# Performance work log

Measured on AMD Instinct MI355X. Metric: run time of the kernel, lower is better.

Reference implementation:

```python
import jax, jax.numpy as jnp
import numpy as np

B, T, C = 16, 2048, 64  # embed_size = 64 (module constant); block_size = T
HEAD = 64


def setup_inputs() -> dict:
    key = jax.random.key(0)
    kx, kq, kk, kv = jax.random.split(key, 4)
    x = jax.random.normal(kx, (B, T, C), dtype=jnp.float32)
    # nn.Linear(embed_size, head_size, bias=False) weights: shape [head_size, embed_size]
    s = 1.0 / np.sqrt(C)
    Wq = jax.random.uniform(kq, (HEAD, C), dtype=jnp.float32, minval=-s, maxval=s)
    Wk = jax.random.uniform(kk, (HEAD, C), dtype=jnp.float32, minval=-s, maxval=s)
    Wv = jax.random.uniform(kv, (HEAD, C), dtype=jnp.float32, minval=-s, maxval=s)
    return {"x": x, "Wq": Wq, "Wk": Wk, "Wv": Wv}


def reference(x, Wq, Wk, Wv):
    Bx, Tx, Cx = x.shape
    q = jnp.einsum('btc,hc->bth', x, Wq)  # [B,T,HEAD]
    k = jnp.einsum('btc,hc->bth', x, Wk)
    v = jnp.einsum('btc,hc->bth', x, Wv)
    scale = Cx ** -0.5  # NOTE: source scales by embed dim C, not head_size
    wei = jnp.einsum('bth,bsh->bts', q, k) * scale  # [B,T,T]
    causal = jnp.tril(jnp.ones((Tx, Tx), dtype=bool))
    wei = jnp.where(causal, wei, -jnp.inf)
    wei = jax.nn.softmax(wei, axis=-1)
    out = jnp.einsum('bts,bsh->bth', wei, v)  # [B,T,HEAD]
    return out
```

## Files before the change

kernel.cpp:

```cpp
#include <hip/hip_runtime.h>


#define Bsz 16
#define Tsz 2048
#define LOG2E 1.44269504088896340736f
#define MFIX 12.0f

typedef __attribute__((ext_vector_type(8))) short bf16x8;
typedef __attribute__((ext_vector_type(4))) short bf16x4;
typedef __attribute__((ext_vector_type(4))) float f32x4;

__device__ inline unsigned short f2bf(float f) {
  union { float f; unsigned u; } v; v.f = f;
  unsigned r = v.u + 0x7fffu + ((v.u >> 16) & 1u);
  return (unsigned short)(r >> 16);
}

__device__ inline bf16x8 pack8(const float* f, float s) {
  bf16x8 o;
#pragma unroll
  for (int i = 0; i < 8; i++) o[i] = (short)f2bf(f[i] * s);
  return o;
}

__device__ inline unsigned pack2_rtz(float a, float b) {
  union { float f; unsigned u; } ua, ub; ua.f = a; ub.f = b;
  return (ua.u >> 16) | (ub.u & 0xffff0000u);
}

__device__ inline float ex2(float x) {
#if __has_builtin(__builtin_amdgcn_exp2f)
  return __builtin_amdgcn_exp2f(x);
#else
  return exp2f(x);
#endif
}

__device__ inline f32x4 pv_mfma(bf16x4 a, bf16x4 b, f32x4 c) {
#if __has_builtin(__builtin_amdgcn_mfma_f32_16x16x16bf16_1k)
  return __builtin_amdgcn_mfma_f32_16x16x16bf16_1k(a, b, c, 0, 0, 0);
#else
  bf16x8 av = {a[0], a[1], a[2], a[3], 0, 0, 0, 0};
  bf16x8 bv = {b[0], b[1], b[2], b[3], 0, 0, 0, 0};
  return __builtin_amdgcn_mfma_f32_16x16x32_bf16(av, bv, c, 0, 0, 0);
#endif
}

__device__ inline void gload_lds16(const unsigned short* g, unsigned short* l) {
  __builtin_amdgcn_global_load_lds(
      (const __attribute__((address_space(1))) unsigned int*)(g),
      (__attribute__((address_space(3))) unsigned int*)(l), 16, 0, 0);
}

__global__ __launch_bounds__(256) void proj_kernel(
    const float* __restrict__ x, const float* __restrict__ Wq,
    const float* __restrict__ Wk, const float* __restrict__ Wv,
    unsigned short* __restrict__ Qs, unsigned short* __restrict__ Kg,
    unsigned short* __restrict__ Vg) {
  __shared__ unsigned short Xb[64 * 72];
  const int b = blockIdx.y, t = blockIdx.x, tbase = t * 64, tid = threadIdx.x;
  const int lane = tid & 63, w = tid >> 6, l15 = lane & 15, quad = lane >> 4;

  bf16x8 bw[3][4][2];
  const float* Ws[3] = {Wq, Wk, Wv};
#pragma unroll
  for (int m = 0; m < 3; m++) {
    const float sc = (m == 0) ? 0.125f * LOG2E : 1.0f;
#pragma unroll
    for (int nb = 0; nb < 4; nb++) {
      const float* wp = Ws[m] + (nb * 16 + l15) * 64 + quad * 8;
      float tf[8];
#pragma unroll
      for (int i = 0; i < 8; i++) tf[i] = wp[i];
      bw[m][nb][0] = pack8(tf, sc);
#pragma unroll
      for (int i = 0; i < 8; i++) tf[i] = wp[32 + i];
      bw[m][nb][1] = pack8(tf, sc);
    }
  }
  {
    const int r = tid >> 2, c0 = (tid & 3) * 16;
    const float* xp = x + ((size_t)b * Tsz + tbase + r) * 64 + c0;
    float tf[16];
#pragma unroll
    for (int i = 0; i < 4; i++) {
      float4 v = *(const float4*)(xp + i * 4);
      tf[i * 4 + 0] = v.x; tf[i * 4 + 1] = v.y; tf[i * 4 + 2] = v.z; tf[i * 4 + 3] = v.w;
    }
    unsigned short* dst = &Xb[r * 72 + c0];
    *(bf16x8*)dst = pack8(tf, 1.0f);
    *(bf16x8*)(dst + 8) = pack8(tf + 8, 1.0f);
  }
  __syncthreads();

  const unsigned short* ap = &Xb[(w * 16 + l15) * 72 + quad * 8];
  const bf16x8 a0 = *(const bf16x8*)ap;
  const bf16x8 a1 = *(const bf16x8*)(ap + 32);

  f32x4 acc[3][4];
#pragma unroll
  for (int m = 0; m < 3; m++)
#pragma unroll
    for (int nb = 0; nb < 4; nb++) {
      f32x4 c = (f32x4){0.f, 0.f, 0.f, 0.f};
      c = __builtin_amdgcn_mfma_f32_16x16x32_bf16(a0, bw[m][nb][0], c, 0, 0, 0);
      c = __builtin_amdgcn_mfma_f32_16x16x32_bf16(a1, bw[m][nb][1], c, 0, 0, 0);
      acc[m][nb] = c;
    }
#pragma unroll
  for (int nb = 0; nb < 4; nb++)
#pragma unroll
    for (int r = 0; r < 4; r++) {
      const size_t row = (size_t)b * Tsz + tbase + w * 16 + quad * 4 + r;
      Qs[row * 64 + nb * 16 + l15] = f2bf(acc[0][nb][r]);
    }
  __syncthreads();
#pragma unroll
  for (int nb = 0; nb < 4; nb++)
#pragma unroll
    for (int r = 0; r < 4; r++)
      Xb[(w * 16 + quad * 4 + r) * 72 + nb * 16 + l15] = f2bf(acc[1][nb][r]);
  __syncthreads();
  const size_t img = ((size_t)b * 32 + t) * 4096;
#pragma unroll
  for (int i = 0; i < 2; i++) {
    const int c = tid + i * 256;
    const int nb = c >> 7, rem = c & 127;
    const int half = rem >> 6, ln = rem & 63;
    const int lr = ln & 15, lq = ln >> 4;
    bf16x8 v = *(const bf16x8*)&Xb[(nb * 16 + lr) * 72 + half * 32 + lq * 8];
    *(bf16x8*)(Kg + img + c * 8) = v;
  }
  __syncthreads();
#pragma unroll
  for (int nb = 0; nb < 4; nb++)
#pragma unroll
    for (int r = 0; r < 4; r++)
      Xb[(nb * 16 + l15) * 72 + quad * 16 + w * 4 + r] = f2bf(acc[2][nb][r]);
  __syncthreads();
#pragma unroll
  for (int i = 0; i < 2; i++) {
    const int c = tid + i * 256;
    const int mb = c >> 7, rem = c & 127;
    const int plane = rem >> 6, ln = rem & 63;
    const int lr = ln & 15, lq = ln >> 4;
    bf16x8 v = *(const bf16x8*)&Xb[(mb * 16 + lr) * 72 + lq * 16 + plane * 8];
    *(bf16x8*)(Vg + img + c * 8) = v;
  }
}

__global__ __launch_bounds__(256) void flash_kernel(
    const unsigned short* __restrict__ Qs, const unsigned short* __restrict__ Kg,
    const unsigned short* __restrict__ Vg, unsigned short* __restrict__ Opart,
    float* __restrict__ Ml) {
  const int b = blockIdx.y;
  const int idx = blockIdx.x;
  int g = 0, base = 0;
  while (idx >= base + 8 * (g + 1)) { base += 8 * (g + 1); g++; }
  const int within = idx - base;
  const int qt = 8 * g + within / (g + 1);
  const int c = within % (g + 1);
  const int qbase = qt * 64;
  const int kstart = c * 512;
  const int kend = min(kstart + 512, qbase + 64);
  const int ntiles = (kend - kstart) >> 6;
  const int t0 = kstart >> 6;

  const int tid = threadIdx.x;
  const int lane = tid & 63, w = tid >> 6;
  const int l15 = lane & 15, quad = lane >> 4;
  const size_t bT = (size_t)b * Tsz;
  const int q = qbase + w * 16 + l15;

  __shared__ unsigned short buf[2][8192];

  const size_t imgbase = (size_t)b * 32 * 4096;
  const int half = (w & 1);
  const unsigned short* gsrc0 =
      ((w < 2) ? Kg : Vg) + imgbase + half * 2048 + lane * 8;
  unsigned short* ldst0 = &buf[0][(w >= 2 ? 4096 : 0) + half * 2048];

  {
    const unsigned short* s = gsrc0 + (size_t)t0 * 4096;
#pragma unroll
    for (int j = 0; j < 4; j++) gload_lds16(s + j * 512, ldst0 + j * 512);
  }

  const unsigned short* Qp = Qs + (bT + q) * 64 + quad * 8;
  const bf16x8 q0 = *(const bf16x8*)Qp;
  const bf16x8 q1 = *(const bf16x8*)(Qp + 32);

  f32x4 O[4];
#pragma unroll
  for (int mb = 0; mb < 4; mb++) O[mb] = (f32x4){0.f, 0.f, 0.f, 0.f};
  float l_acc = 0.f;

  __syncthreads();

  for (int i = 0; i < ntiles; i++) {
    const unsigned short* kb = buf[i & 1];
    const unsigned short* vb = buf[i & 1] + 4096;
    if (i + 1 < ntiles) {
      const unsigned short* s = gsrc0 + (size_t)(t0 + i + 1) * 4096;
      unsigned short* d = ldst0 + ((i + 1) & 1) * 8192;
#pragma unroll
      for (int j = 0; j < 4; j++) gload_lds16(s + j * 512, d + j * 512);
    }
    bf16x8 k0[4], k1[4];
#pragma unroll
    for (int nb = 0; nb < 4; nb++) {
      k0[nb] = *(const bf16x8*)(kb + nb * 1024 + lane * 8);
      k1[nb] = *(const bf16x8*)(kb + nb * 1024 + 512 + lane * 8);
    }
    bf16x4 vf[4][4];
#pragma unroll
    for (int mb = 0; mb < 4; mb++) {
      bf16x8 va = *(const bf16x8*)(vb + mb * 1024 + lane * 8);
      bf16x8 vb2 = *(const bf16x8*)(vb + mb * 1024 + 512 + lane * 8);
      vf[mb][0] = (bf16x4){va[0], va[1], va[2], va[3]};
      vf[mb][1] = (bf16x4){va[4], va[5], va[6], va[7]};
      vf[mb][2] = (bf16x4){vb2[0], vb2[1], vb2[2], vb2[3]};
      vf[mb][3] = (bf16x4){vb2[4], vb2[5], vb2[6], vb2[7]};
    }
    f32x4 S[4];
#pragma unroll
    for (int nb = 0; nb < 4; nb++) {
      f32x4 cc = (f32x4){0.f, 0.f, 0.f, 0.f};
      cc = __builtin_amdgcn_mfma_f32_16x16x32_bf16(k0[nb], q0, cc, 0, 0, 0);
      cc = __builtin_amdgcn_mfma_f32_16x16x32_bf16(k1[nb], q1, cc, 0, 0, 0);
      S[nb] = cc;
    }
    const int kt = kstart + i * 64;
    float p[4][4];
    if (kt == qbase) {
#pragma unroll
      for (int nb = 0; nb < 4; nb++)
#pragma unroll
        for (int r = 0; r < 4; r++) {
          const int s = kt + nb * 16 + quad * 4 + r;
          float pv = ex2(S[nb][r] - MFIX);
          p[nb][r] = (s > q) ? 0.f : pv;
        }
    } else {
#pragma unroll
      for (int nb = 0; nb < 4; nb++)
#pragma unroll
        for (int r = 0; r < 4; r++) p[nb][r] = ex2(S[nb][r] - MFIX);
    }
#pragma unroll
    for (int nb = 0; nb < 4; nb++)
#pragma unroll
      for (int r = 0; r < 4; r++) l_acc += p[nb][r];
    bf16x4 pf[4];
#pragma unroll
    for (int nb = 0; nb < 4; nb++) {
      union { unsigned u[2]; bf16x4 v; } tt;
      tt.u[0] = pack2_rtz(p[nb][0], p[nb][1]);
      tt.u[1] = pack2_rtz(p[nb][2], p[nb][3]);
      pf[nb] = tt.v;
    }
#pragma unroll
    for (int nb = 0; nb < 4; nb++)
#pragma unroll
      for (int mb = 0; mb < 4; mb++) O[mb] = pv_mfma(vf[mb][nb], pf[nb], O[mb]);
    __syncthreads();
  }

  const int pidx = b * 80 + idx;
  unsigned short* Op = Opart + (size_t)pidx * 4096 + (w * 16 + l15) * 64 + quad * 4;
#pragma unroll
  for (int mb = 0; mb < 4; mb++) {
    union { unsigned u[2]; bf16x4 v; } tt;
    tt.u[0] = (unsigned)f2bf(O[mb][0]) | ((unsigned)f2bf(O[mb][1]) << 16);
    tt.u[1] = (unsigned)f2bf(O[mb][2]) | ((unsigned)f2bf(O[mb][3]) << 16);
    *(bf16x4*)(Op + mb * 16) = tt.v;
  }
  l_acc += __shfl_xor(l_acc, 16, 64);
  l_acc += __shfl_xor(l_acc, 32, 64);
  if (quad == 0) Ml[(size_t)pidx * 64 + w * 16 + l15] = l_acc;
}

__global__ __launch_bounds__(256) void merge_kernel(
    const unsigned short* __restrict__ Opart, const float* __restrict__ Ml,
    float* __restrict__ out) {
  const int qt = blockIdx.x, b = blockIdx.y;
  const int g = qt >> 3;
  const int pbase = b * 80 + 4 * g * (g + 1) + (qt - 8 * g) * (g + 1);
  const int nch = g + 1;
  const int tid = threadIdx.x;
  const int ql = tid >> 2;
  const int h0 = (tid & 3) * 16;

  float acc[16];
#pragma unroll
  for (int i = 0; i < 16; i++) acc[i] = 0.f;
  float ld = 0.f;
  for (int c = 0; c < nch; c++) {
    const int pidx = pbase + c;
    ld += Ml[(size_t)pidx * 64 + ql];
    const unsigned short* Op = Opart + (size_t)pidx * 4096 + ql * 64 + h0;
    bf16x8 v0 = *(const bf16x8*)Op;
    bf16x8 v1 = *(const bf16x8*)(Op + 8);
#pragma unroll
    for (int i = 0; i < 8; i++) {
      union { unsigned u; float f; } t;
      t.u = ((unsigned)(unsigned short)v0[i]) << 16;
      acc[i] += t.f;
      t.u = ((unsigned)(unsigned short)v1[i]) << 16;
      acc[8 + i] += t.f;
    }
  }
  const float rd = 1.0f / ld;
  float* op = out + ((size_t)b * Tsz + qt * 64 + ql) * 64 + h0;
#pragma unroll
  for (int i = 0; i < 4; i++) {
    f32x4 v = {acc[i * 4] * rd, acc[i * 4 + 1] * rd, acc[i * 4 + 2] * rd,
               acc[i * 4 + 3] * rd};
    *(f32x4*)(op + i * 4) = v;
  }
}

extern "C" void kernel_launch(void* const* d_in, const int* in_sizes, int n_in,
                              void* d_out, int out_size, void* d_ws, size_t ws_size,
                              hipStream_t stream) {
  const float* x = (const float*)d_in[0];
  const float* Wq = (const float*)d_in[1];
  const float* Wk = (const float*)d_in[2];
  const float* Wv = (const float*)d_in[3];

  unsigned short* Qs = (unsigned short*)d_ws;
  unsigned short* Kg = Qs + (size_t)Bsz * Tsz * 64;
  unsigned short* Vg = Kg + (size_t)Bsz * Tsz * 64;
  unsigned short* Opart = Vg + (size_t)Bsz * Tsz * 64;
  float* Ml = (float*)(Opart + (size_t)Bsz * 80 * 4096);

  dim3 pgrid(Tsz / 64, Bsz);
  proj_kernel<<<pgrid, 256, 0, stream>>>(x, Wq, Wk, Wv, Qs, Kg, Vg);
  dim3 fgrid(80, Bsz);
  flash_kernel<<<fgrid, 256, 0, stream>>>(Qs, Kg, Vg, Opart, Ml);
  dim3 mgrid(32, Bsz);
  merge_kernel<<<mgrid, 256, 0, stream>>>(Opart, Ml, (float*)d_out);
}
```

Baseline: 108.2 us.

## Fuse split-K merge into flash kernel via last-block atomic counter

Removes the separate merge kernel launch. Each flash block writes its partial result, bumps a per-query-tile atomic counter (reset in the projection kernel), and the last-arriving block performs the merge and writes the final fp32 output. Query tiles with a single chunk now write normalized output directly, skipping the bf16 partial round-trip. This saves a launch and tail gap but adds fences, an atomic and a serialized merge at the end of some blocks.

```diff
diff --git a/kernel.cpp b/kernel.cpp
--- a/kernel.cpp
+++ b/kernel.cpp
@@ -56,10 +56,14 @@
     const float* __restrict__ x, const float* __restrict__ Wq,
     const float* __restrict__ Wk, const float* __restrict__ Wv,
     unsigned short* __restrict__ Qs, unsigned short* __restrict__ Kg,
-    unsigned short* __restrict__ Vg) {
+    unsigned short* __restrict__ Vg, unsigned int* __restrict__ cnt) {
   __shared__ unsigned short Xb[64 * 72];
   const int b = blockIdx.y, t = blockIdx.x, tbase = t * 64, tid = threadIdx.x;
   const int lane = tid & 63, w = tid >> 6, l15 = lane & 15, quad = lane >> 4;
+
+  if (tid == 0)
+    __hip_atomic_store(&cnt[b * 32 + t], 0u, __ATOMIC_RELAXED,
+                       __HIP_MEMORY_SCOPE_AGENT);
 
   bf16x8 bw[3][4][2];
   const float* Ws[3] = {Wq, Wk, Wv};
@@ -152,7 +156,8 @@
 __global__ __launch_bounds__(256) void flash_kernel(
     const unsigned short* __restrict__ Qs, const unsigned short* __restrict__ Kg,
     const unsigned short* __restrict__ Vg, unsigned short* __restrict__ Opart,
-    float* __restrict__ Ml) {
+    float* __restrict__ Ml, unsigned int* __restrict__ cnt,
+    float* __restrict__ out) {
   const int b = blockIdx.y;
   const int idx = blockIdx.x;
   int g = 0, base = 0;
@@ -160,6 +165,7 @@
   const int within = idx - base;
   const int qt = 8 * g + within / (g + 1);
   const int c = within % (g + 1);
+  const int nch = g + 1;
   const int qbase = qt * 64;
   const int kstart = c * 512;
   const int kend = min(kstart + 512, qbase + 64);
@@ -266,6 +272,22 @@
     __syncthreads();
   }
 
+  l_acc += __shfl_xor(l_acc, 16, 64);
+  l_acc += __shfl_xor(l_acc, 32, 64);
+
+  if (nch == 1) {
+    const float rl = 1.0f / l_acc;
+    float* op = out + (bT + q) * 64 + quad * 4;
+#pragma unroll
+    for (int mb = 0; mb < 4; mb++) {
+      f32x4 o;
+#pragma unroll
+      for (int r = 0; r < 4; r++) o[r] = O[mb][r] * rl;
+      *(f32x4*)(op + mb * 16) = o;
+    }
+    return;
+  }
+
   const int pidx = b * 80 + idx;
   unsigned short* Op = Opart + (size_t)pidx * 4096 + (w * 16 + l15) * 64 + quad * 4;
 #pragma unroll
@@ -275,32 +297,31 @@
     tt.u[1] = (unsigned)f2bf(O[mb][2]) | ((unsigned)f2bf(O[mb][3]) << 16);
     *(bf16x4*)(Op + mb * 16) = tt.v;
   }
-  l_acc += __shfl_xor(l_acc, 16, 64);
-  l_acc += __shfl_xor(l_acc, 32, 64);
   if (quad == 0) Ml[(size_t)pidx * 64 + w * 16 + l15] = l_acc;
-}
-
-__global__ __launch_bounds__(256) void merge_kernel(
-    const unsigned short* __restrict__ Opart, const float* __restrict__ Ml,
-    float* __restrict__ out) {
-  const int qt = blockIdx.x, b = blockIdx.y;
-  const int g = qt >> 3;
-  const int pbase = b * 80 + 4 * g * (g + 1) + (qt - 8 * g) * (g + 1);
-  const int nch = g + 1;
-  const int tid = threadIdx.x;
+
+  __threadfence();
+  volatile int* flag = (volatile int*)&buf[0][0];
+  if (tid == 0) {
+    unsigned old = atomicAdd(&cnt[b * 32 + qt], 1u);
+    *flag = (old == (unsigned)(nch - 1)) ? 1 : 0;
+  }
+  __syncthreads();
+  if (*flag == 0) return;
+  __threadfence();
+
+  const int pbase = pidx - c;
   const int ql = tid >> 2;
   const int h0 = (tid & 3) * 16;
-
   float acc[16];
 #pragma unroll
   for (int i = 0; i < 16; i++) acc[i] = 0.f;
   float ld = 0.f;
-  for (int c = 0; c < nch; c++) {
-    const int pidx = pbase + c;
-    ld += Ml[(size_t)pidx * 64 + ql];
-    const unsigned short* Op = Opart + (size_t)pidx * 4096 + ql * 64 + h0;
-    bf16x8 v0 = *(const bf16x8*)Op;
-    bf16x8 v1 = *(const bf16x8*)(Op + 8);
+  for (int cc = 0; cc < nch; cc++) {
+    const int pi = pbase + cc;
+    ld += Ml[(size_t)pi * 64 + ql];
+    const unsigned short* Rp = Opart + (size_t)pi * 4096 + ql * 64 + h0;
+    bf16x8 v0 = *(const bf16x8*)Rp;
+    bf16x8 v1 = *(const bf16x8*)(Rp + 8);
 #pragma unroll
     for (int i = 0; i < 8; i++) {
       union { unsigned u; float f; } t;
@@ -311,7 +332,7 @@
     }
   }
   const float rd = 1.0f / ld;
-  float* op = out + ((size_t)b * Tsz + qt * 64 + ql) * 64 + h0;
+  float* op = out + (bT + qbase + ql) * 64 + h0;
 #pragma unroll
   for (int i = 0; i < 4; i++) {
     f32x4 v = {acc[i * 4] * rd, acc[i * 4 + 1] * rd, acc[i * 4 + 2] * rd,
@@ -333,11 +354,11 @@
   unsigned short* Vg = Kg + (size_t)Bsz * Tsz * 64;
   unsigned short* Opart = Vg + (size_t)Bsz * Tsz * 64;
   float* Ml = (float*)(Opart + (size_t)Bsz * 80 * 4096);
+  unsigned int* cnt = (unsigned int*)(Ml + (size_t)Bsz * 80 * 64);
 
   dim3 pgrid(Tsz / 64, Bsz);
-  proj_kernel<<<pgrid, 256, 0, stream>>>(x, Wq, Wk, Wv, Qs, Kg, Vg);
+  proj_kernel<<<pgrid, 256, 0, stream>>>(x, Wq, Wk, Wv, Qs, Kg, Vg, cnt);
   dim3 fgrid(80, Bsz);
-  flash_kernel<<<fgrid, 256, 0, stream>>>(Qs, Kg, Vg, Opart, Ml);
-  dim3 mgrid(32, Bsz);
-  merge_kernel<<<mgrid, 256, 0, stream>>>(Opart, Ml, (float*)d_out);
-}
+  flash_kernel<<<fgrid, 256, 0, stream>>>(Qs, Kg, Vg, Opart, Ml, cnt,
+                                          (float*)d_out);
+}
```

New measurement: 324.6 us. +200.0%, slower.
